# Kernel tuning notes

Measured on AMD Instinct MI355X. Metric: run time of the kernel, lower is better.

Reference implementation:

```python
import jax, jax.numpy as jnp
import numpy as np

HEAD_DIM = 64
HIDDEN_SIZE = 2880
NUM_HEADS = 64
NUM_KV_HEADS = 8
INPUT_SIZE = 2 * HIDDEN_SIZE


def _rotate_half(x):
    x1, x2 = jnp.split(x, 2, axis=-1)
    return jnp.concatenate([-x2, x1], axis=-1)


def _apply_rotary_emb(x, cos, sin):
    return x * cos + _rotate_half(x) * sin


def setup_inputs() -> dict:
    key = jax.random.key(0)
    ks = jax.random.split(key, 7)
    B, S = 1, 2048
    hidden_states = jax.random.normal(ks[0], (B, S, INPUT_SIZE), dtype=jnp.float32)
    cos = jax.random.uniform(ks[1], (1, 1, S, HEAD_DIM), dtype=jnp.float32)
    sin = jax.random.uniform(ks[2], (1, 1, S, HEAD_DIM), dtype=jnp.float32)
    sc = 1.0 / np.sqrt(INPUT_SIZE)
    wq = jax.random.normal(ks[3], (INPUT_SIZE, NUM_HEADS * HEAD_DIM), dtype=jnp.float32) * sc
    wk = jax.random.normal(ks[4], (INPUT_SIZE, NUM_KV_HEADS * HEAD_DIM), dtype=jnp.float32) * sc
    wv = jax.random.normal(ks[5], (INPUT_SIZE, NUM_KV_HEADS * HEAD_DIM), dtype=jnp.float32) * sc
    wo = jax.random.normal(ks[6], (NUM_HEADS * HEAD_DIM, HIDDEN_SIZE), dtype=jnp.float32) * (1.0 / np.sqrt(NUM_HEADS * HEAD_DIM))
    return {"hidden_states": hidden_states, "cos": cos, "sin": sin,
            "wq": wq, "wk": wk, "wv": wv, "wo": wo}


def reference(hidden_states, cos, sin, wq, wk, wv, wo):
    B, S, _ = hidden_states.shape
    # projections -> [B, H, S, D]
    q = (hidden_states @ wq).reshape(B, S, NUM_HEADS, HEAD_DIM).transpose(0, 2, 1, 3)
    k = (hidden_states @ wk).reshape(B, S, NUM_KV_HEADS, HEAD_DIM).transpose(0, 2, 1, 3)
    v = (hidden_states @ wv).reshape(B, S, NUM_KV_HEADS, HEAD_DIM).transpose(0, 2, 1, 3)
    q = _apply_rotary_emb(q, cos, sin)
    k = _apply_rotary_emb(k, cos, sin)
    # GQA expand KV heads: [B, Hkv, S, D] -> [B, H, S, D]
    groups = NUM_HEADS // NUM_KV_HEADS
    k = jnp.repeat(k, groups, axis=1)
    v = jnp.repeat(v, groups, axis=1)
    scale = 1.0 / np.sqrt(HEAD_DIM).astype(np.float32)
    attn = jnp.einsum('bhqd,bhkd->bhqk', q, k) * scale  # [B,H,S,S]
    attn = jax.nn.softmax(attn.astype(jnp.float32), axis=-1).astype(q.dtype)
    out = jnp.einsum('bhqk,bhkd->bhqd', attn, v)
    out = out.transpose(0, 2, 1, 3).reshape(B, S, NUM_HEADS * HEAD_DIM)
    return out @ wo
```

## Files before the change

### kernel.cpp

```cpp
#include <hip/hip_runtime.h>
#include <hip/hip_bf16.h>

#define SEQ   2048
#define INSZ  5760
#define NQ    4096
#define NKV   512
#define NQKV  5120
#define HQ    64
#define HKV   8
#define HD    64
#define HID   2880
#define HIDP  2944

typedef __attribute__((ext_vector_type(8))) short bf16x8;
typedef __attribute__((ext_vector_type(4))) float f32x4;

__device__ __forceinline__ unsigned short f2bf(float x) {
  __hip_bfloat16 b = __float2bfloat16(x);
  return __builtin_bit_cast(unsigned short, b);
}
__device__ __forceinline__ float bf2f(unsigned short u) {
  return __bfloat162float(__builtin_bit_cast(__hip_bfloat16, u));
}

__global__ void k_convert(const float* __restrict__ src, unsigned short* __restrict__ dst, int n) {
  int stride = gridDim.x * blockDim.x * 4;
  for (int idx = (blockIdx.x * blockDim.x + threadIdx.x) * 4; idx < n; idx += stride) {
    float4 v = *(const float4*)(src + idx);
    ushort4 o;
    o.x = f2bf(v.x); o.y = f2bf(v.y); o.z = f2bf(v.z); o.w = f2bf(v.w);
    *(ushort4*)(dst + idx) = o;
  }
}

__global__ void k_tconv(const float* __restrict__ src, unsigned short* __restrict__ dst,
                        int K, int N) {
  __shared__ float tile[32][33];
  int k0 = blockIdx.x * 32, n0 = blockIdx.y * 32;
  int r = threadIdx.x >> 5, c = threadIdx.x & 31;
#pragma unroll
  for (int i = 0; i < 4; i++) {
    int row = i * 8 + r;
    float v = (n0 + c < N) ? src[(size_t)(k0 + row) * N + n0 + c] : 0.f;
    tile[row][c] = v;
  }
  __syncthreads();
#pragma unroll
  for (int i = 0; i < 4; i++) {
    int n = n0 + i * 8 + r;
    dst[(size_t)n * K + k0 + c] = f2bf(tile[c][i * 8 + r]);
  }
}

template <typename OutT>
__global__ __launch_bounds__(256) void k_gemm_bt(
    const unsigned short* __restrict__ A,
    const unsigned short* __restrict__ BT,
    OutT* __restrict__ C, int Kdim, int Ncols, int ldc) {
  __shared__ unsigned short sA[128 * 32];
  __shared__ unsigned short sB[128 * 32];
  int tid = threadIdx.x, wid = tid >> 6, lane = tid & 63;
  int bm = blockIdx.x, bn = blockIdx.y;
  const unsigned short* Ab = A + (size_t)bm * 128 * Kdim;
  const unsigned short* Bb = BT + (size_t)bn * 128 * Kdim;
  f32x4 acc[4][4];
#pragma unroll
  for (int i = 0; i < 4; i++)
#pragma unroll
    for (int j = 0; j < 4; j++) acc[i][j] = f32x4{0.f, 0.f, 0.f, 0.f};
  int wr = (wid >> 1) * 64, wc = (wid & 1) * 64;
  int srow = lane >> 2;
  int selem = (lane & 3) * 8;
  int rbase = lane & 15, koff = (lane >> 4) * 8;

  for (int kt = 0; kt < Kdim; kt += 32) {
    __syncthreads();
#pragma unroll
    for (int ch2 = 0; ch2 < 2; ++ch2) {
      int chunk = wid * 2 + ch2;
      const unsigned short* ga = Ab + (size_t)(chunk * 16 + srow) * Kdim + kt + selem;
      const unsigned short* gb = Bb + (size_t)(chunk * 16 + srow) * Kdim + kt + selem;
      __builtin_amdgcn_global_load_lds(
          (const __attribute__((address_space(1))) void*)ga,
          (__attribute__((address_space(3))) void*)(sA + chunk * 512), 16, 0, 0);
      __builtin_amdgcn_global_load_lds(
          (const __attribute__((address_space(1))) void*)gb,
          (__attribute__((address_space(3))) void*)(sB + chunk * 512), 16, 0, 0);
    }
    __syncthreads();
    bf16x8 a[4], b[4];
#pragma unroll
    for (int i = 0; i < 4; i++)
      a[i] = *(const bf16x8*)(sA + (wr + i * 16 + rbase) * 32 + koff);
#pragma unroll
    for (int j = 0; j < 4; j++)
      b[j] = *(const bf16x8*)(sB + (wc + j * 16 + rbase) * 32 + koff);
#pragma unroll
    for (int i = 0; i < 4; i++)
#pragma unroll
      for (int j = 0; j < 4; j++)
        acc[i][j] = __builtin_amdgcn_mfma_f32_16x16x32_bf16(a[i], b[j], acc[i][j], 0, 0, 0);
  }
  int rw = (lane >> 4) * 4, cl = lane & 15;
#pragma unroll
  for (int i = 0; i < 4; i++)
#pragma unroll
    for (int j = 0; j < 4; j++) {
      int col = bn * 128 + wc + j * 16 + cl;
      if (col < Ncols) {
#pragma unroll
        for (int r = 0; r < 4; r++) {
          int row = bm * 128 + wr + i * 16 + rw + r;
          float v = acc[i][j][r];
          if constexpr (sizeof(OutT) == 2)
            C[(size_t)row * ldc + col] = (OutT)f2bf(v);
          else
            C[(size_t)row * ldc + col] = v;
        }
      }
    }
}

__global__ void k_rope(unsigned short* __restrict__ qkv, const float* __restrict__ cosb,
                       const float* __restrict__ sinb) {
  int s = blockIdx.x;
  const float* cs = cosb + s * HD;
  const float* sn = sinb + s * HD;
  unsigned short* row = qkv + (size_t)s * NQKV;
  for (int idx = threadIdx.x; idx < (HQ + HKV) * 32; idx += blockDim.x) {
    int head = idx >> 5, dp = idx & 31;
    unsigned short* base = row + (head < HQ ? head * 64 : NQ + (head - HQ) * 64);
    float x1 = bf2f(base[dp]), x2 = bf2f(base[dp + 32]);
    float o1 = x1 * cs[dp] - x2 * sn[dp];
    float o2 = x2 * cs[dp + 32] + x1 * sn[dp + 32];
    base[dp] = f2bf(o1);
    base[dp + 32] = f2bf(o2);
  }
}

__global__ void k_vtrans(const unsigned short* __restrict__ qkv, unsigned short* __restrict__ vt) {
  __shared__ unsigned short tile[64 * 66];
  int st = blockIdx.x, hk = blockIdx.y;
  int s0 = st * 64, t = threadIdx.x;
#pragma unroll
  for (int i = 0; i < 16; i++) {
    int e = i * 256 + t;
    int sl = e >> 6, d = e & 63;
    tile[d * 66 + sl] = qkv[(size_t)(s0 + sl) * NQKV + NQ + NKV + hk * 64 + d];
  }
  __syncthreads();
#pragma unroll
  for (int i = 0; i < 16; i++) {
    int e = i * 256 + t;
    int d = e >> 6, sl = e & 63;
    vt[(size_t)(hk * 64 + d) * SEQ + s0 + sl] = tile[d * 66 + sl];
  }
}

__global__ __launch_bounds__(256) void k_attn(
    const unsigned short* __restrict__ qkv, const unsigned short* __restrict__ vt,
    unsigned short* __restrict__ out) {
  __shared__ unsigned short sK[2][64 * 64];
  __shared__ unsigned short sV[2][64 * 64];
  __shared__ unsigned short sP[4 * 16 * 64];
  int tid = threadIdx.x, wid = tid >> 6, lane = tid & 63;
  int head = blockIdx.x, qt = blockIdx.y;
  int hkv = head >> 3;
  int q0 = qt * 64 + wid * 16;
  int rbase = lane & 15, lg = lane >> 4;
  int koff = lg * 8;

  const unsigned short* qrow = qkv + (size_t)(q0 + rbase) * NQKV + head * 64;
  bf16x8 qa0 = *(const bf16x8*)(qrow + koff);
  bf16x8 qa1 = *(const bf16x8*)(qrow + 32 + koff);

  int r8 = lane >> 3;
  int srcslot = ((lane & 7) ^ r8) * 16;

  int sw = rbase & 7;
  int off0 = rbase * 128 + (lg ^ sw) * 16;
  int off1 = rbase * 128 + ((lg + 4) ^ sw) * 16;

  f32x4 o[4];
#pragma unroll
  for (int i = 0; i < 4; i++) o[i] = f32x4{0.f, 0.f, 0.f, 0.f};
  float m[4] = {-3e38f, -3e38f, -3e38f, -3e38f};
  float lp[4] = {0.f, 0.f, 0.f, 0.f};
  const float SL2 = 0.125f * 1.44269504f;
  char* myP = (char*)(sP + wid * 16 * 64);

  int sbase = rbase >> 3;
  int pw_base[4], pw_x[4];
#pragma unroll
  for (int j = 0; j < 4; j++) {
    int prow = lg * 4 + j;
    pw_base[j] = prow * 128 + (rbase & 7) * 2;
    pw_x[j] = prow & 7;
  }

#define STAGE_KV(buf, kv)                                                            \
  {                                                                                  \
    _Pragma("unroll") for (int ch = 0; ch < 2; ++ch) {                               \
      int r0 = (wid * 2 + ch) * 8;                                                   \
      const char* gk =                                                               \
          (const char*)(qkv + (size_t)((kv) + r0 + r8) * NQKV + NQ + hkv * 64) +     \
          srcslot;                                                                   \
      __builtin_amdgcn_global_load_lds(                                              \
          (const __attribute__((address_space(1))) void*)gk,                         \
          (__attribute__((address_space(3))) void*)(&sK[buf][r0 * 64]), 16, 0, 0);   \
      const char* gv =                                                               \
          (const char*)(vt + (size_t)(hkv * 64 + r0 + r8) * SEQ + (kv)) + srcslot;   \
      __builtin_amdgcn_global_load_lds(                                              \
          (const __attribute__((address_space(1))) void*)gv,                         \
          (__attribute__((address_space(3))) void*)(&sV[buf][r0 * 64]), 16, 0, 0);   \
    }                                                                                \
  }

  STAGE_KV(0, 0);
  __syncthreads();
  int cur = 0;

  for (int kvt = 0; kvt < SEQ / 64; ++kvt) {
    if (kvt + 1 < SEQ / 64) STAGE_KV(cur ^ 1, (kvt + 1) * 64);

    const char* kb = (const char*)&sK[cur][0];
    const char* vb = (const char*)&sV[cur][0];

    f32x4 sc[4];
#pragma unroll
    for (int c = 0; c < 4; c++) sc[c] = f32x4{0.f, 0.f, 0.f, 0.f};
#pragma unroll
    for (int c = 0; c < 4; c++) {
      bf16x8 kb0 = *(const bf16x8*)(kb + c * 2048 + off0);
      bf16x8 kb1 = *(const bf16x8*)(kb + c * 2048 + off1);
      sc[c] = __builtin_amdgcn_mfma_f32_16x16x32_bf16(qa0, kb0, sc[c], 0, 0, 0);
      sc[c] = __builtin_amdgcn_mfma_f32_16x16x32_bf16(qa1, kb1, sc[c], 0, 0, 0);
    }

    float t2[4];
#pragma unroll
    for (int j = 0; j < 4; j++) {
      float t = fmaxf(fmaxf(sc[0][j], sc[1][j]), fmaxf(sc[2][j], sc[3][j])) * SL2;
#pragma unroll
      for (int d = 1; d < 16; d <<= 1) t = fmaxf(t, __shfl_xor(t, d, 64));
      t2[j] = t;
    }
    bool need = (t2[0] > m[0] + 8.f) || (t2[1] > m[1] + 8.f) ||
                (t2[2] > m[2] + 8.f) || (t2[3] > m[3] + 8.f);
    if (__any(need)) {
      float corr[4];
#pragma unroll
      for (int j = 0; j < 4; j++) {
        float mn = fmaxf(m[j], t2[j]);
        corr[j] = exp2f(m[j] - mn);
        m[j] = mn;
        lp[j] *= corr[j];
      }
#pragma unroll
      for (int dt = 0; dt < 4; dt++) {
        f32x4 t = o[dt];
        t[0] *= corr[0]; t[1] *= corr[1]; t[2] *= corr[2]; t[3] *= corr[3];
        o[dt] = t;
      }
    }

    float psum[4] = {0.f, 0.f, 0.f, 0.f};
#pragma unroll
    for (int c = 0; c < 4; c++) {
#pragma unroll
      for (int j = 0; j < 4; j++) {
        float p = exp2f(sc[c][j] * SL2 - m[j]);
        psum[j] += p;
        *(unsigned short*)(myP + pw_base[j] + ((c * 2 + sbase) ^ pw_x[j]) * 16) = f2bf(p);
      }
    }
#pragma unroll
    for (int j = 0; j < 4; j++) lp[j] += psum[j];

    bf16x8 pa0 = *(const bf16x8*)(myP + off0);
    bf16x8 pa1 = *(const bf16x8*)(myP + off1);
#pragma unroll
    for (int dt = 0; dt < 4; dt++) {
      bf16x8 vb0 = *(const bf16x8*)(vb + dt * 2048 + off0);
      bf16x8 vb1 = *(const bf16x8*)(vb + dt * 2048 + off1);
      o[dt] = __builtin_amdgcn_mfma_f32_16x16x32_bf16(pa0, vb0, o[dt], 0, 0, 0);
      o[dt] = __builtin_amdgcn_mfma_f32_16x16x32_bf16(pa1, vb1, o[dt], 0, 0, 0);
    }

    __syncthreads();
    cur ^= 1;
  }

#pragma unroll
  for (int j = 0; j < 4; j++) {
#pragma unroll
    for (int d = 1; d < 16; d <<= 1) lp[j] += __shfl_xor(lp[j], d, 64);
    lp[j] = 1.0f / lp[j];
  }
#pragma unroll
  for (int dt = 0; dt < 4; dt++)
#pragma unroll
    for (int j = 0; j < 4; j++) {
      int row = q0 + lg * 4 + j;
      int col = head * 64 + dt * 16 + rbase;
      out[(size_t)row * NQ + col] = f2bf(o[dt][j] * lp[j]);
    }
#undef STAGE_KV
}

extern "C" void kernel_launch(void* const* d_in, const int* in_sizes, int n_in,
                              void* d_out, int out_size, void* d_ws, size_t ws_size,
                              hipStream_t stream) {
  const float* hidden = (const float*)d_in[0];
  const float* cosb = (const float*)d_in[1];
  const float* sinb = (const float*)d_in[2];
  const float* wq = (const float*)d_in[3];
  const float* wk = (const float*)d_in[4];
  const float* wv = (const float*)d_in[5];
  const float* wo = (const float*)d_in[6];
  float* out = (float*)d_out;

  unsigned short* hb = (unsigned short*)d_ws;
  unsigned short* qkv = hb + (size_t)SEQ * INSZ;
  unsigned short* wqkvT = qkv + (size_t)SEQ * NQKV;
  unsigned short* woT = wqkvT + (size_t)NQKV * INSZ;
  unsigned short* vt = woT + (size_t)HIDP * NQ;
  unsigned short* attn = vt + (size_t)NKV * SEQ;

  k_convert<<<dim3(1024), dim3(256), 0, stream>>>(hidden, hb, SEQ * INSZ);
  k_tconv<<<dim3(INSZ / 32, NQ / 32), dim3(256), 0, stream>>>(wq, wqkvT, INSZ, NQ);
  k_tconv<<<dim3(INSZ / 32, NKV / 32), dim3(256), 0, stream>>>(
      wk, wqkvT + (size_t)NQ * INSZ, INSZ, NKV);
  k_tconv<<<dim3(INSZ / 32, NKV / 32), dim3(256), 0, stream>>>(
      wv, wqkvT + (size_t)(NQ + NKV) * INSZ, INSZ, NKV);
  k_tconv<<<dim3(NQ / 32, HIDP / 32), dim3(256), 0, stream>>>(wo, woT, NQ, HID);

  k_gemm_bt<unsigned short><<<dim3(SEQ / 128, NQKV / 128), dim3(256), 0, stream>>>(
      hb, wqkvT, qkv, INSZ, NQKV, NQKV);
  k_rope<<<dim3(SEQ), dim3(256), 0, stream>>>(qkv, cosb, sinb);
  k_vtrans<<<dim3(SEQ / 64, HKV), dim3(256), 0, stream>>>(qkv, vt);
  k_attn<<<dim3(HQ, SEQ / 64), dim3(256), 0, stream>>>(qkv, vt, attn);
  k_gemm_bt<float><<<dim3(SEQ / 128, (HID + 127) / 128), dim3(256), 0, stream>>>(
      attn, woT, out, NQ, HID, HID);
}
```

Measured before the change: 766.5 us.

## Rewrite attention with 32x32 MFMA, register-resident P, and XCD-aware GEMM swizzle

The attention kernel now has each wave handle 32 query rows and uses 32x32x16 MFMA with transposed operands, so scores land in registers already laid out for the P·V product. P is packed to bf16 with hardware converts and exchanged across lane halves with shuffles instead of going through LDS. Exponentials use v_exp_f32 directly, and output is staged through LDS for coalesced 16-byte stores. The GEMMs also remap block indices per XCD to improve L2 locality. In exchange, the attention kernel launches half as many blocks and carries more register pressure.

```diff
diff --git a/kernel.cpp b/kernel.cpp
--- a/kernel.cpp
+++ b/kernel.cpp
@@ -14,6 +14,8 @@
 
 typedef __attribute__((ext_vector_type(8))) short bf16x8;
 typedef __attribute__((ext_vector_type(4))) float f32x4;
+typedef __attribute__((ext_vector_type(16))) float f32x16;
+typedef unsigned int u32;
 
 __device__ __forceinline__ unsigned short f2bf(float x) {
   __hip_bfloat16 b = __float2bfloat16(x);
@@ -21,6 +23,16 @@
 }
 __device__ __forceinline__ float bf2f(unsigned short u) {
   return __bfloat162float(__builtin_bit_cast(__hip_bfloat16, u));
+}
+__device__ __forceinline__ float exp2_hw(float x) {
+  float r;
+  asm("v_exp_f32 %0, %1" : "=v"(r) : "v"(x));
+  return r;
+}
+__device__ __forceinline__ u32 cvt_pk_bf16(float lo, float hi) {
+  u32 r;
+  asm("v_cvt_pk_bf16_f32 %0, %1, %2" : "=v"(r) : "v"(lo), "v"(hi));
+  return r;
 }
 
 __global__ void k_convert(const float* __restrict__ src, unsigned short* __restrict__ dst, int n) {
@@ -60,7 +72,13 @@
   __shared__ unsigned short sA[128 * 32];
   __shared__ unsigned short sB[128 * 32];
   int tid = threadIdx.x, wid = tid >> 6, lane = tid & 63;
-  int bm = blockIdx.x, bn = blockIdx.y;
+  int gx = gridDim.x;
+  int nwg = gx * gridDim.y;
+  int lin = blockIdx.y * gx + blockIdx.x;
+  int qn = nwg >> 3, rn = nwg & 7;
+  int xcd = lin & 7, idx = lin >> 3;
+  int swz = (xcd < rn ? xcd * (qn + 1) : rn * (qn + 1) + (xcd - rn) * qn) + idx;
+  int bm = swz % gx, bn = swz / gx;
   const unsigned short* Ab = A + (size_t)bm * 128 * Kdim;
   const unsigned short* Bb = BT + (size_t)bn * 128 * Kdim;
   f32x4 acc[4][4];
@@ -160,43 +178,24 @@
 __global__ __launch_bounds__(256) void k_attn(
     const unsigned short* __restrict__ qkv, const unsigned short* __restrict__ vt,
     unsigned short* __restrict__ out) {
-  __shared__ unsigned short sK[2][64 * 64];
-  __shared__ unsigned short sV[2][64 * 64];
-  __shared__ unsigned short sP[4 * 16 * 64];
+  __shared__ unsigned short smem[16384];
   int tid = threadIdx.x, wid = tid >> 6, lane = tid & 63;
   int head = blockIdx.x, qt = blockIdx.y;
   int hkv = head >> 3;
-  int q0 = qt * 64 + wid * 16;
-  int rbase = lane & 15, lg = lane >> 4;
-  int koff = lg * 8;
-
-  const unsigned short* qrow = qkv + (size_t)(q0 + rbase) * NQKV + head * 64;
-  bf16x8 qa0 = *(const bf16x8*)(qrow + koff);
-  bf16x8 qa1 = *(const bf16x8*)(qrow + 32 + koff);
+  int q = lane & 31, h = lane >> 5;
+  int q0w = qt * 128 + wid * 32;
+  const float SL2 = 0.125f * 1.44269504f;
+
+  bf16x8 qf[4];
+  {
+    const unsigned short* qrow = qkv + (size_t)(q0w + q) * NQKV + head * 64 + h * 8;
+#pragma unroll
+    for (int ks = 0; ks < 4; ks++) qf[ks] = *(const bf16x8*)(qrow + ks * 16);
+  }
 
   int r8 = lane >> 3;
   int srcslot = ((lane & 7) ^ r8) * 16;
-
-  int sw = rbase & 7;
-  int off0 = rbase * 128 + (lg ^ sw) * 16;
-  int off1 = rbase * 128 + ((lg + 4) ^ sw) * 16;
-
-  f32x4 o[4];
-#pragma unroll
-  for (int i = 0; i < 4; i++) o[i] = f32x4{0.f, 0.f, 0.f, 0.f};
-  float m[4] = {-3e38f, -3e38f, -3e38f, -3e38f};
-  float lp[4] = {0.f, 0.f, 0.f, 0.f};
-  const float SL2 = 0.125f * 1.44269504f;
-  char* myP = (char*)(sP + wid * 16 * 64);
-
-  int sbase = rbase >> 3;
-  int pw_base[4], pw_x[4];
-#pragma unroll
-  for (int j = 0; j < 4; j++) {
-    int prow = lg * 4 + j;
-    pw_base[j] = prow * 128 + (rbase & 7) * 2;
-    pw_x[j] = prow & 7;
-  }
+  int sw = q & 7;
 
 #define STAGE_KV(buf, kv)                                                            \
   {                                                                                  \
@@ -207,14 +206,22 @@
           srcslot;                                                                   \
       __builtin_amdgcn_global_load_lds(                                              \
           (const __attribute__((address_space(1))) void*)gk,                         \
-          (__attribute__((address_space(3))) void*)(&sK[buf][r0 * 64]), 16, 0, 0);   \
+          (__attribute__((address_space(3))) void*)(smem + (buf)*4096 + r0 * 64),    \
+          16, 0, 0);                                                                 \
       const char* gv =                                                               \
           (const char*)(vt + (size_t)(hkv * 64 + r0 + r8) * SEQ + (kv)) + srcslot;   \
       __builtin_amdgcn_global_load_lds(                                              \
           (const __attribute__((address_space(1))) void*)gv,                         \
-          (__attribute__((address_space(3))) void*)(&sV[buf][r0 * 64]), 16, 0, 0);   \
+          (__attribute__((address_space(3))) void*)(smem + 8192 + (buf)*4096 +       \
+                                                    r0 * 64),                        \
+          16, 0, 0);                                                                 \
     }                                                                                \
   }
+
+  f32x16 o0, o1;
+#pragma unroll
+  for (int r = 0; r < 16; r++) { o0[r] = 0.f; o1[r] = 0.f; }
+  float m = -3e38f, lp = 0.f;
 
   STAGE_KV(0, 0);
   __syncthreads();
@@ -222,89 +229,122 @@
 
   for (int kvt = 0; kvt < SEQ / 64; ++kvt) {
     if (kvt + 1 < SEQ / 64) STAGE_KV(cur ^ 1, (kvt + 1) * 64);
-
-    const char* kb = (const char*)&sK[cur][0];
-    const char* vb = (const char*)&sV[cur][0];
-
-    f32x4 sc[4];
-#pragma unroll
-    for (int c = 0; c < 4; c++) sc[c] = f32x4{0.f, 0.f, 0.f, 0.f};
-#pragma unroll
-    for (int c = 0; c < 4; c++) {
-      bf16x8 kb0 = *(const bf16x8*)(kb + c * 2048 + off0);
-      bf16x8 kb1 = *(const bf16x8*)(kb + c * 2048 + off1);
-      sc[c] = __builtin_amdgcn_mfma_f32_16x16x32_bf16(qa0, kb0, sc[c], 0, 0, 0);
-      sc[c] = __builtin_amdgcn_mfma_f32_16x16x32_bf16(qa1, kb1, sc[c], 0, 0, 0);
-    }
-
-    float t2[4];
-#pragma unroll
-    for (int j = 0; j < 4; j++) {
-      float t = fmaxf(fmaxf(sc[0][j], sc[1][j]), fmaxf(sc[2][j], sc[3][j])) * SL2;
-#pragma unroll
-      for (int d = 1; d < 16; d <<= 1) t = fmaxf(t, __shfl_xor(t, d, 64));
-      t2[j] = t;
-    }
-    bool need = (t2[0] > m[0] + 8.f) || (t2[1] > m[1] + 8.f) ||
-                (t2[2] > m[2] + 8.f) || (t2[3] > m[3] + 8.f);
-    if (__any(need)) {
-      float corr[4];
-#pragma unroll
-      for (int j = 0; j < 4; j++) {
-        float mn = fmaxf(m[j], t2[j]);
-        corr[j] = exp2f(m[j] - mn);
-        m[j] = mn;
-        lp[j] *= corr[j];
-      }
-#pragma unroll
-      for (int dt = 0; dt < 4; dt++) {
-        f32x4 t = o[dt];
-        t[0] *= corr[0]; t[1] *= corr[1]; t[2] *= corr[2]; t[3] *= corr[3];
-        o[dt] = t;
-      }
-    }
-
-    float psum[4] = {0.f, 0.f, 0.f, 0.f};
-#pragma unroll
-    for (int c = 0; c < 4; c++) {
-#pragma unroll
-      for (int j = 0; j < 4; j++) {
-        float p = exp2f(sc[c][j] * SL2 - m[j]);
-        psum[j] += p;
-        *(unsigned short*)(myP + pw_base[j] + ((c * 2 + sbase) ^ pw_x[j]) * 16) = f2bf(p);
-      }
-    }
-#pragma unroll
-    for (int j = 0; j < 4; j++) lp[j] += psum[j];
-
-    bf16x8 pa0 = *(const bf16x8*)(myP + off0);
-    bf16x8 pa1 = *(const bf16x8*)(myP + off1);
-#pragma unroll
-    for (int dt = 0; dt < 4; dt++) {
-      bf16x8 vb0 = *(const bf16x8*)(vb + dt * 2048 + off0);
-      bf16x8 vb1 = *(const bf16x8*)(vb + dt * 2048 + off1);
-      o[dt] = __builtin_amdgcn_mfma_f32_16x16x32_bf16(pa0, vb0, o[dt], 0, 0, 0);
-      o[dt] = __builtin_amdgcn_mfma_f32_16x16x32_bf16(pa1, vb1, o[dt], 0, 0, 0);
+    const char* kb = (const char*)(smem + cur * 4096);
+    const char* vb = (const char*)(smem + 8192 + cur * 4096);
+
+    f32x16 st0, st1;
+#pragma unroll
+    for (int r = 0; r < 16; r++) { st0[r] = 0.f; st1[r] = 0.f; }
+    {
+      bf16x8 kf[4];
+#pragma unroll
+      for (int ks = 0; ks < 4; ks++)
+        kf[ks] = *(const bf16x8*)(kb + q * 128 + (((2 * ks + h) ^ sw) << 4));
+#pragma unroll
+      for (int ks = 0; ks < 4; ks++)
+        st0 = __builtin_amdgcn_mfma_f32_32x32x16_bf16(kf[ks], qf[ks], st0, 0, 0, 0);
+#pragma unroll
+      for (int ks = 0; ks < 4; ks++)
+        kf[ks] = *(const bf16x8*)(kb + (32 + q) * 128 + (((2 * ks + h) ^ sw) << 4));
+#pragma unroll
+      for (int ks = 0; ks < 4; ks++)
+        st1 = __builtin_amdgcn_mfma_f32_32x32x16_bf16(kf[ks], qf[ks], st1, 0, 0, 0);
+    }
+
+    float tmx[16];
+#pragma unroll
+    for (int r = 0; r < 16; r++) tmx[r] = fmaxf(st0[r], st1[r]);
+#pragma unroll
+    for (int s = 8; s >= 1; s >>= 1)
+#pragma unroll
+      for (int r = 0; r < 8; r++)
+        if (r < s) tmx[r] = fmaxf(tmx[r], tmx[r + s]);
+    float mx = fmaxf(tmx[0], __shfl_xor(tmx[0], 32, 64));
+    float t2 = mx * SL2;
+
+    if (__any(t2 > m + 8.f)) {
+      float mn = fmaxf(m, t2);
+      float corr = exp2_hw(m - mn);
+      m = mn;
+      lp *= corr;
+#pragma unroll
+      for (int r = 0; r < 16; r++) { o0[r] *= corr; o1[r] *= corr; }
+    }
+
+    float psa[4] = {0.f, 0.f, 0.f, 0.f};
+#pragma unroll
+    for (int r = 0; r < 16; r++) {
+      float e0 = exp2_hw(fmaf(st0[r], SL2, -m));
+      float e1 = exp2_hw(fmaf(st1[r], SL2, -m));
+      st0[r] = e0; st1[r] = e1;
+      psa[r & 3] += e0 + e1;
+    }
+    lp += (psa[0] + psa[1]) + (psa[2] + psa[3]);
+
+    u32 pk[16];
+#pragma unroll
+    for (int w = 0; w < 8; w++) {
+      pk[w] = cvt_pk_bf16(st0[2 * w], st0[2 * w + 1]);
+      pk[8 + w] = cvt_pk_bf16(st1[2 * w], st1[2 * w + 1]);
+    }
+
+    bf16x8 pf[4];
+#pragma unroll
+    for (int ks = 0; ks < 4; ks++) {
+      int base = 8 * (ks >> 1) + 4 * (ks & 1);
+      u32 wA0 = pk[base], wA1 = pk[base + 1], wB0 = pk[base + 2], wB1 = pk[base + 3];
+      u32 keep0 = h ? wB0 : wA0, keep1 = h ? wB1 : wA1;
+      u32 send0 = h ? wA0 : wB0, send1 = h ? wA1 : wB1;
+      u32 rc0 = (u32)__shfl_xor((int)send0, 32, 64);
+      u32 rc1 = (u32)__shfl_xor((int)send1, 32, 64);
+      union { u32 w[4]; bf16x8 v; } u;
+      u.w[0] = h ? rc0 : keep0;
+      u.w[1] = h ? rc1 : keep1;
+      u.w[2] = h ? keep0 : rc0;
+      u.w[3] = h ? keep1 : rc1;
+      pf[ks] = u.v;
+    }
+
+    {
+      bf16x8 vf[4];
+#pragma unroll
+      for (int ks = 0; ks < 4; ks++)
+        vf[ks] = *(const bf16x8*)(vb + q * 128 + (((2 * ks + h) ^ sw) << 4));
+#pragma unroll
+      for (int ks = 0; ks < 4; ks++)
+        o0 = __builtin_amdgcn_mfma_f32_32x32x16_bf16(vf[ks], pf[ks], o0, 0, 0, 0);
+#pragma unroll
+      for (int ks = 0; ks < 4; ks++)
+        vf[ks] = *(const bf16x8*)(vb + (32 + q) * 128 + (((2 * ks + h) ^ sw) << 4));
+#pragma unroll
+      for (int ks = 0; ks < 4; ks++)
+        o1 = __builtin_amdgcn_mfma_f32_32x32x16_bf16(vf[ks], pf[ks], o1, 0, 0, 0);
     }
 
     __syncthreads();
     cur ^= 1;
   }
 
-#pragma unroll
-  for (int j = 0; j < 4; j++) {
-#pragma unroll
-    for (int d = 1; d < 16; d <<= 1) lp[j] += __shfl_xor(lp[j], d, 64);
-    lp[j] = 1.0f / lp[j];
-  }
-#pragma unroll
-  for (int dt = 0; dt < 4; dt++)
-#pragma unroll
-    for (int j = 0; j < 4; j++) {
-      int row = q0 + lg * 4 + j;
-      int col = head * 64 + dt * 16 + rbase;
-      out[(size_t)row * NQ + col] = f2bf(o[dt][j] * lp[j]);
-    }
+  float lpt = lp + __shfl_xor(lp, 32, 64);
+  float inv = 1.0f / lpt;
+
+  unsigned short* ot = smem + wid * (32 * 72);
+#pragma unroll
+  for (int w = 0; w < 8; w++) {
+    int reg = 2 * w;
+    int dbase = (reg & 3) + 8 * (reg >> 2) + 4 * h;
+    u32 p0 = cvt_pk_bf16(o0[reg] * inv, o0[reg + 1] * inv);
+    u32 p1 = cvt_pk_bf16(o1[reg] * inv, o1[reg + 1] * inv);
+    *(u32*)(ot + q * 72 + dbase) = p0;
+    *(u32*)(ot + q * 72 + 32 + dbase) = p1;
+  }
+  __syncthreads();
+  int row = lane >> 1, halfc = lane & 1;
+  const unsigned short* src = ot + row * 72 + halfc * 32;
+  unsigned short* dst = out + (size_t)(q0w + row) * NQ + head * 64 + halfc * 32;
+#pragma unroll
+  for (int c = 0; c < 4; c++)
+    *(bf16x8*)(dst + c * 8) = *(const bf16x8*)(src + c * 8);
 #undef STAGE_KV
 }
 
@@ -339,7 +379,7 @@
       hb, wqkvT, qkv, INSZ, NQKV, NQKV);
   k_rope<<<dim3(SEQ), dim3(256), 0, stream>>>(qkv, cosb, sinb);
   k_vtrans<<<dim3(SEQ / 64, HKV), dim3(256), 0, stream>>>(qkv, vt);
-  k_attn<<<dim3(HQ, SEQ / 64), dim3(256), 0, stream>>>(qkv, vt, attn);
+  k_attn<<<dim3(HQ, SEQ / 128), dim3(256), 0, stream>>>(qkv, vt, attn);
   k_gemm_bt<float><<<dim3(SEQ / 128, (HID + 127) / 128), dim3(256), 0, stream>>>(
       attn, woT, out, NQ, HID, HID);
 }
```

Measured after the change: 673.1 us. 12.2% less time.
